# Performance work log

Hardware: AMD Instinct MI355X
Metric: run time of the kernel (lower is better)

Reference implementation:

```python
import jax, jax.numpy as jnp
import numpy as np

B, N, H, DH, M = 4, 4096, 16, 64, 266  # batch, seq, heads, dim_head, nb_features
D = H * DH                              # hidden_size = 1024
EPS_FAVOR = 1e-4
EPS_LN = 1e-5


def _gaussian_orthogonal_matrix(m, d, rng):
    # performer_pytorch gaussian_orthogonal_random_matrix, scaling=0
    nb_blocks = int(np.ceil(m / d))
    blocks = []
    for _ in range(nb_blocks):
        q, _ = np.linalg.qr(rng.standard_normal((d, d)))
        blocks.append(q.T)
    W = np.concatenate(blocks, axis=0)[:m]
    multiplier = np.linalg.norm(rng.standard_normal((m, d)), axis=1)
    return (multiplier[:, None] * W).astype(np.float32)


def setup_inputs() -> dict:
    key = jax.random.key(0)
    ks = jax.random.split(key, 6)
    s = D ** -0.5
    rng = np.random.default_rng(0)
    return {
        "hidden_states": jax.random.normal(ks[0], (B, N, D), jnp.float32),
        "Wq": jax.random.normal(ks[1], (D, D), jnp.float32) * s,
        "Wk": jax.random.normal(ks[2], (D, D), jnp.float32) * s,
        "Wv": jax.random.normal(ks[3], (D, D), jnp.float32) * s,
        "Wo": jax.random.normal(ks[4], (D, D), jnp.float32) * s,
        "bo": jnp.zeros((D,), jnp.float32),
        "proj": jnp.asarray(_gaussian_orthogonal_matrix(M, DH, rng)),  # [M, DH]
        "gamma": jnp.ones((D,), jnp.float32),
        "beta": jnp.zeros((D,), jnp.float32),
    }


def _softmax_kernel(x, proj, is_query):
    # x: [B,H,N,DH]; FAVOR+ positive random features for the softmax kernel
    dn = DH ** -0.25
    ratio = proj.shape[0] ** -0.5
    xs = x * dn
    xd = jnp.einsum('bhnd,md->bhnm', xs, proj)            # [B,H,N,M]
    diag = 0.5 * jnp.sum(xs * xs, axis=-1, keepdims=True)  # ||x||^2 / (2 sqrt(d))
    if is_query:
        stab = jnp.max(xd, axis=-1, keepdims=True)
    else:
        stab = jnp.max(xd, axis=(-2, -1), keepdims=True)
    stab = jax.lax.stop_gradient(stab)
    return ratio * (jnp.exp(xd - diag - stab) + EPS_FAVOR)


def reference(hidden_states, Wq, Wk, Wv, Wo, bo, proj, gamma, beta):
    x = hidden_states
    # qkv projections (no bias), split heads -> [B,H,N,DH]
    def heads(t):
        return t.reshape(B, N, H, DH).transpose(0, 2, 1, 3)
    q = heads(x @ Wq)
    k = heads(x @ Wk)
    v = heads(x @ Wv)

    qf = _softmax_kernel(q, proj, True)    # [B,H,N,M]
    kf = _softmax_kernel(k, proj, False)   # [B,H,N,M]

    # non-causal linear attention
    k_sum = jnp.sum(kf, axis=-2)                              # [B,H,M]
    d_inv = 1.0 / jnp.einsum('bhnm,bhm->bhn', qf, k_sum)      # [B,H,N]
    ctx = jnp.einsum('bhnm,bhnd->bhmd', kf, v)                # [B,H,M,DH]
    out = jnp.einsum('bhmd,bhnm,bhn->bhnd', ctx, qf, d_inv)   # [B,H,N,DH]

    out = out.transpose(0, 2, 1, 3).reshape(B, N, D)
    out = out @ Wo + bo

    # residual + LayerNorm
    y = x + out
    mu = jnp.mean(y, axis=-1, keepdims=True)
    var = jnp.mean((y - mu) ** 2, axis=-1, keepdims=True)
    return (y - mu) / jnp.sqrt(var + EPS_LN) * gamma + beta
```

## Files before the change

kernel.cpp:

```cpp
#include <hip/hip_runtime.h>
#include <hip/hip_bf16.h>
#include <math.h>

#define Bb 4
#define Nn 4096
#define Hh 16
#define DHh 64
#define Mm 266
#define Dd 1024
#define BHh (Bb*Hh)

#define DN_SCALE 0.35355339059327373f
#define RATIO 0.06131393394849658f
#define EPS_FAVOR 1e-4f
#define EPS_LN 1e-5f

typedef __attribute__((ext_vector_type(8))) short frag_t;
typedef __attribute__((ext_vector_type(4))) short sh4;
typedef __attribute__((ext_vector_type(4))) float f32x4;

__device__ __forceinline__ ushort f2bf(float f) {
    unsigned u = __float_as_uint(f);
    return (ushort)((u + 0x7FFFu + ((u >> 16) & 1u)) >> 16);
}
__device__ __forceinline__ float bf2f(ushort h) {
    return __uint_as_float(((unsigned)h) << 16);
}
__device__ __forceinline__ unsigned fenc(float f) {
    unsigned u = __float_as_uint(f);
    return (u & 0x80000000u) ? ~u : (u | 0x80000000u);
}
__device__ __forceinline__ float fdec(unsigned e) {
    unsigned u = (e & 0x80000000u) ? (e ^ 0x80000000u) : ~e;
    return __uint_as_float(u);
}
__device__ __forceinline__ void gld16(const void* g, void* l) {
    __builtin_amdgcn_global_load_lds((const __attribute__((address_space(1))) unsigned int*)g,
                                     (__attribute__((address_space(3))) unsigned int*)l, 16, 0, 0);
}

#define SYNC_LDS() do {                                             \
        asm volatile("s_waitcnt lgkmcnt(0)" ::: "memory");          \
        __builtin_amdgcn_sched_barrier(0);                          \
        __builtin_amdgcn_s_barrier();                               \
        __builtin_amdgcn_sched_barrier(0);                          \
    } while (0)

__global__ __launch_bounds__(256) void conv_x_kernel(const float* __restrict__ x,
                                                     ushort* __restrict__ xb) {
    size_t i = ((size_t)blockIdx.x * 256 + threadIdx.x) * 8;
    float4 f0 = *(const float4*)(x + i);
    float4 f1 = *(const float4*)(x + i + 4);
    uint4 o;
    o.x = (unsigned)f2bf(f0.x) | ((unsigned)f2bf(f0.y) << 16);
    o.y = (unsigned)f2bf(f0.z) | ((unsigned)f2bf(f0.w) << 16);
    o.z = (unsigned)f2bf(f1.x) | ((unsigned)f2bf(f1.y) << 16);
    o.w = (unsigned)f2bf(f1.z) | ((unsigned)f2bf(f1.w) << 16);
    *(uint4*)(xb + i) = o;
}

__global__ __launch_bounds__(256) void conv_wt_kernel(
    const float* __restrict__ Wq, const float* __restrict__ Wk,
    const float* __restrict__ Wv, const float* __restrict__ Wo,
    ushort* __restrict__ Tq, ushort* __restrict__ Tk,
    ushort* __restrict__ Tv, ushort* __restrict__ To) {
    const int z = blockIdx.z;
    const float* W = z == 0 ? Wq : z == 1 ? Wk : z == 2 ? Wv : Wo;
    ushort* WT = z == 0 ? Tq : z == 1 ? Tk : z == 2 ? Tv : To;
    __shared__ float tls[64][65];
    const int tid = threadIdx.x;
    const int n0 = blockIdx.x * 64, k0 = blockIdx.y * 64;
    const int r = tid >> 2, seg = tid & 3;
#pragma unroll
    for (int i = 0; i < 4; ++i) {
        float4 f = *(const float4*)(W + (size_t)(k0 + r) * 1024 + n0 + seg * 16 + i * 4);
        tls[r][seg * 16 + i * 4 + 0] = f.x;
        tls[r][seg * 16 + i * 4 + 1] = f.y;
        tls[r][seg * 16 + i * 4 + 2] = f.z;
        tls[r][seg * 16 + i * 4 + 3] = f.w;
    }
    __syncthreads();
    const int nl = tid >> 2;
#pragma unroll
    for (int i = 0; i < 16; ++i)
        WT[(size_t)(n0 + nl) * 1024 + k0 + seg * 16 + i] = f2bf(tls[seg * 16 + i][nl]);
}

__global__ __launch_bounds__(256) void conv_proj_kernel(const float* __restrict__ proj,
                                                        ushort* __restrict__ pb) {
    const int idx = blockIdx.x * 256 + threadIdx.x;
    const int m = idx >> 6, k = idx & 63;
    float v = (m < Mm) ? proj[m * 64 + k] : 0.f;
    ushort hi = f2bf(v);
    float lo = v - bf2f(hi);
    pb[m * 128 + k] = hi;
    pb[m * 128 + 64 + k] = f2bf(lo);
}

__global__ __launch_bounds__(256) void diag_kernel(const ushort* __restrict__ kb,
                                                   float* __restrict__ dg) {
    const size_t i = (size_t)blockIdx.x * 256 + threadIdx.x;
    const ushort* p = kb + i * 64;
    float s = 0.f;
#pragma unroll
    for (int seg = 0; seg < 8; ++seg) {
        frag_t a = *(const frag_t*)(p + seg * 8);
#pragma unroll
        for (int j = 0; j < 8; ++j) { float f = bf2f((ushort)a[j]); s += f * f; }
    }
    dg[i] = 0.5f * s;
}

__global__ __launch_bounds__(256) void ctx2bt_kernel(const float* __restrict__ ctx,
                                                     ushort* __restrict__ cT) {
    const int mc = blockIdx.x;
    const int bh = blockIdx.y;
    const int tid = threadIdx.x;
    __shared__ float tls[64][65];
    const int r = tid >> 2, cs = tid & 3;
    const int gm = mc * 64 + r;
#pragma unroll
    for (int i = 0; i < 4; ++i) {
        float4 f = {0.f, 0.f, 0.f, 0.f};
        if (gm < Mm) f = *(const float4*)(ctx + ((size_t)bh * Mm + gm) * 64 + cs * 16 + i * 4);
        tls[r][cs * 16 + i * 4 + 0] = f.x;
        tls[r][cs * 16 + i * 4 + 1] = f.y;
        tls[r][cs * 16 + i * 4 + 2] = f.z;
        tls[r][cs * 16 + i * 4 + 3] = f.w;
    }
    __syncthreads();
    const int d = tid >> 2, ms = tid & 3;
    unsigned hi[8], lo[8];
#pragma unroll
    for (int j = 0; j < 8; ++j) {
        float v0 = tls[ms * 16 + j * 2][d];
        float v1 = tls[ms * 16 + j * 2 + 1][d];
        ushort h0 = f2bf(v0), h1 = f2bf(v1);
        ushort l0 = f2bf(v0 - bf2f(h0)), l1 = f2bf(v1 - bf2f(h1));
        hi[j] = (unsigned)h0 | ((unsigned)h1 << 16);
        lo[j] = (unsigned)l0 | ((unsigned)l1 << 16);
    }
    size_t base = (size_t)bh * 40960 + (size_t)d * 640 + mc * 64 + ms * 16;
    uint4 a = {hi[0], hi[1], hi[2], hi[3]};
    uint4 b = {hi[4], hi[5], hi[6], hi[7]};
    uint4 c = {lo[0], lo[1], lo[2], lo[3]};
    uint4 e = {lo[4], lo[5], lo[6], lo[7]};
    *(uint4*)(cT + base) = a;
    *(uint4*)(cT + base + 8) = b;
    *(uint4*)(cT + base + 320) = c;
    *(uint4*)(cT + base + 328) = e;
}

__global__ __launch_bounds__(512, 2) void gemm256(
    const ushort* __restrict__ A,
    const ushort* __restrict__ W0, const ushort* __restrict__ W1, const ushort* __restrict__ W2,
    ushort* __restrict__ o0, ushort* __restrict__ o1, ushort* __restrict__ o2,
    const float* __restrict__ bo, const float* __restrict__ xres, float* __restrict__ yres,
    int mode)
{
    __shared__ ushort smem[65536];
    const int tid = threadIdx.x;
    const int lane = tid & 63, w = tid >> 6;
    const int q = lane >> 4, m16 = lane & 15;
    const int wm = w >> 2, wn = w & 3;
    const int row0 = blockIdx.x * 256, col0 = blockIdx.y * 256;
    const int z = blockIdx.z;
    const ushort* WT = (mode == 0) ? (z == 0 ? W0 : z == 1 ? W1 : W2) : W0;

    const int srow = tid >> 2, sseg = tid & 3;
    const int ksw = (sseg ^ ((srow >> 1) & 3)) * 8;
    const int dst = tid * 8;
    const int sq  = (q ^ ((m16 >> 1) & 3)) * 8;

#define STG(T_) do {                                                          \
        int s0_ = (2 * (T_)) & 7, s1_ = (2 * (T_) + 1) & 7;                   \
        gld16(A  + (size_t)(row0 + srow) * 1024 + (T_) * 32 + ksw,            \
              smem + s0_ * 8192 + dst);                                       \
        gld16(WT + (size_t)(col0 + srow) * 1024 + (T_) * 32 + ksw,            \
              smem + s0_ * 8192 + 4096 + dst);                                \
        gld16(A  + (size_t)(row0 + 128 + srow) * 1024 + (T_) * 32 + ksw,      \
              smem + s1_ * 8192 + dst);                                       \
        gld16(WT + (size_t)(col0 + 128 + srow) * 1024 + (T_) * 32 + ksw,      \
              smem + s1_ * 8192 + 4096 + dst);                                \
    } while (0)

    f32x4 acc[8][4];
#pragma unroll
    for (int i = 0; i < 8; ++i)
#pragma unroll
        for (int j = 0; j < 4; ++j) acc[i][j] = (f32x4){0.f, 0.f, 0.f, 0.f};

    STG(0);
    STG(1);
    STG(2);

    for (int kt = 0; kt < 32; ++kt) {
        if (kt < 30)       { asm volatile("s_waitcnt vmcnt(8)" ::: "memory"); }
        else if (kt == 30) { asm volatile("s_waitcnt vmcnt(4)" ::: "memory"); }
        else               { asm volatile("s_waitcnt vmcnt(0)" ::: "memory"); }
        __builtin_amdgcn_sched_barrier(0);
        __builtin_amdgcn_s_barrier();
        __builtin_amdgcn_sched_barrier(0);

        if (kt + 3 < 32) STG(kt + 3);

        const ushort* As_ = smem + (((2 * kt + wm) & 7) * 8192);
        const ushort* Bs_ = smem + (((2 * kt + (wn >> 1)) & 7) * 8192) + 4096;
        frag_t af[8], bf[4];
#pragma unroll
        for (int i = 0; i < 8; ++i)
            af[i] = *(const frag_t*)&As_[(i * 16 + m16) * 32 + sq];
#pragma unroll
        for (int j = 0; j < 4; ++j)
            bf[j] = *(const frag_t*)&Bs_[((wn & 1) * 64 + j * 16 + m16) * 32 + sq];

        __builtin_amdgcn_s_setprio(1);
#pragma unroll
        for (int i = 0; i < 8; ++i)
#pragma unroll
            for (int j = 0; j < 4; ++j)
                acc[i][j] = __builtin_amdgcn_mfma_f32_16x16x32_bf16(af[i], bf[j], acc[i][j], 0, 0, 0);
        __builtin_amdgcn_s_setprio(0);
    }
#undef STG

    const int b = row0 >> 12;
    if (mode == 0) {
        if (z == 2) {
#pragma unroll
            for (int i = 0; i < 8; ++i)
#pragma unroll
                for (int j = 0; j < 4; ++j) {
                    int col = col0 + wn * 64 + j * 16 + m16;
                    size_t rowbase = ((size_t)((b << 4) + (col >> 6)) * 64 + (col & 63)) * 4096;
                    int n = (row0 & 4095) + wm * 128 + i * 16 + q * 4;
                    sh4 pk;
#pragma unroll
                    for (int r = 0; r < 4; ++r) pk[r] = (short)f2bf(acc[i][j][r]);
                    *(sh4*)(o2 + rowbase + n) = pk;
                }
        } else {
            ushort* outp = (z == 0) ? o0 : o1;
#pragma unroll
            for (int c = 0; c < 4; ++c) {
                __builtin_amdgcn_s_barrier();
                if (wm == (c >> 1)) {
#pragma unroll
                    for (int i2 = 0; i2 < 4; ++i2) {
                        int i = (c & 1) * 4 + i2;
#pragma unroll
                        for (int j = 0; j < 4; ++j)
#pragma unroll
                            for (int r = 0; r < 4; ++r)
                                smem[(i2 * 16 + q * 4 + r) * 264 + wn * 64 + j * 16 + m16] =
                                    f2bf(acc[i][j][r] * DN_SCALE);
                    }
                }
                __builtin_amdgcn_s_barrier();
#pragma unroll
                for (int it = 0; it < 4; ++it) {
                    int idx = it * 512 + tid;
                    int lr = idx >> 5, ch = idx & 31;
                    frag_t v = *(const frag_t*)&smem[lr * 264 + ch * 8];
                    int n = (row0 & 4095) + c * 64 + lr;
                    int h = (col0 >> 6) + (ch >> 3);
                    int dh = (ch & 7) * 8;
                    *(frag_t*)(outp + ((size_t)((b << 4) + h) * 4096 + n) * 64 + dh) = v;
                }
            }
        }
    } else {
#pragma unroll
        for (int i = 0; i < 8; ++i)
#pragma unroll
            for (int j = 0; j < 4; ++j)
#pragma unroll
                for (int r = 0; r < 4; ++r) {
                    int row = row0 + wm * 128 + i * 16 + q * 4 + r;
                    int col = col0 + wn * 64 + j * 16 + m16;
                    size_t off = (size_t)row * 1024 + col;
                    yres[off] = acc[i][j][r] + bo[col] + xres[off];
                }
    }
}

__global__ __launch_bounds__(256) void kstab_mfma_kernel(
    const ushort* __restrict__ kb, const ushort* __restrict__ pb,
    unsigned* __restrict__ stab_enc)
{
    const int n0 = blockIdx.x * 256;
    const int bh = blockIdx.y;
    const int tid = threadIdx.x;
    const int lane = tid & 63, w = tid >> 6;
    const int q = lane >> 4, m16 = lane & 15;

    __shared__ ushort ks_s[256 * 72];
    __shared__ ushort pj_s[64 * 72];

#pragma unroll
    for (int t = 0; t < 8; ++t) {
        int idx = tid + t * 256;
        int r = idx >> 3, s = idx & 7;
        *(frag_t*)&ks_s[r * 72 + s * 8] =
            *(const frag_t*)(kb + ((size_t)bh * Nn + n0 + r) * 64 + s * 8);
    }
    __syncthreads();

    frag_t aq[4][2];
#pragma unroll
    for (int g = 0; g < 4; ++g)
#pragma unroll
        for (int s = 0; s < 2; ++s)
            aq[g][s] = *(const frag_t*)&ks_s[(w * 64 + g * 16 + m16) * 72 + s * 32 + q * 8];

    float mx = -3.0e38f;
#pragma unroll
    for (int mc = 0; mc < 5; ++mc) {
        __syncthreads();
#pragma unroll
        for (int t = 0; t < 2; ++t) {
            int idx = tid + t * 256;
            int r = idx >> 3, cc = idx & 7;
            *(frag_t*)&pj_s[r * 72 + cc * 8] =
                *(const frag_t*)(pb + ((size_t)mc * 64 + r) * 128 + cc * 8);
        }
        __syncthreads();
#pragma unroll
        for (int tm = 0; tm < 4; ++tm) {
            const int t = mc * 4 + tm;
            if (t > 16) continue;
            frag_t bh0 = *(const frag_t*)&pj_s[(tm * 16 + m16) * 72 + q * 8];
            frag_t bh1 = *(const frag_t*)&pj_s[(tm * 16 + m16) * 72 + 32 + q * 8];
            bool v = (t < 16) || (m16 < 10);
#pragma unroll
            for (int g = 0; g < 4; ++g) {
                f32x4 sa = (f32x4){0.f, 0.f, 0.f, 0.f};
                sa = __builtin_amdgcn_mfma_f32_16x16x32_bf16(aq[g][0], bh0, sa, 0, 0, 0);
                sa = __builtin_amdgcn_mfma_f32_16x16x32_bf16(aq[g][1], bh1, sa, 0, 0, 0);
                if (v) {
#pragma unroll
                    for (int r = 0; r < 4; ++r) mx = fmaxf(mx, sa[r]);
                }
            }
        }
    }
    mx = fmaxf(mx, __shfl_xor(mx, 1));
    mx = fmaxf(mx, __shfl_xor(mx, 2));
    mx = fmaxf(mx, __shfl_xor(mx, 4));
    mx = fmaxf(mx, __shfl_xor(mx, 8));
    mx = fmaxf(mx, __shfl_xor(mx, 16));
    mx = fmaxf(mx, __shfl_xor(mx, 32));
    if (lane == 0) atomicMax(stab_enc + bh, fenc(mx));
}

__global__ __launch_bounds__(256) void ctx_mfma_kernel(
    const ushort* __restrict__ kb, const ushort* __restrict__ vT,
    const ushort* __restrict__ pb, const float* __restrict__ diagk,
    const unsigned* __restrict__ stab_enc,
    float* __restrict__ ctx, float* __restrict__ ksum)
{
    const int m0 = blockIdx.x * 64;
    const int nb = blockIdx.y;
    const int bh = blockIdx.z;
    const int tid = threadIdx.x;
    const int lane = tid & 63, w = tid >> 6;
    const int q = lane >> 4, m16 = lane & 15;
    const float kst = fdec(stab_enc[bh]);

    __shared__ ushort ks_s[32 * 72];
    __shared__ ushort pj_s[64 * 136];
    __shared__ ushort kf_s[64 * 40];
    __shared__ ushort vt_s[64 * 40];
    __shared__ float  diag_s[32];

    for (int u = tid; u < 1024; u += 256) {
        int r = u >> 4, c = (u & 15) * 8;
        *(frag_t*)&pj_s[r * 136 + c] = *(const frag_t*)(pb + (size_t)(m0 + r) * 128 + c);
    }

    f32x4 acc_c[4];
#pragma unroll
    for (int j = 0; j < 4; ++j) acc_c[j] = (f32x4){0.f, 0.f, 0.f, 0.f};
    float ksacc[2] = {0.f, 0.f};

    const int tn  = w & 1;
    const int tmb = (w >> 1) * 2;

    const int srow_k = tid >> 3, sseg_k = tid & 7;
    const int srow_v = tid >> 2, sseg_v = tid & 3;
    const size_t kbase = ((size_t)bh * Nn + nb * 1024 + srow_k) * 64 + sseg_k * 8;
    const size_t vbase = ((size_t)bh * 64 + srow_v) * Nn + nb * 1024 + sseg_v * 8;
    const float* dgp = diagk + (size_t)bh * Nn + nb * 1024;

    frag_t kreg = *(const frag_t*)(kb + kbase);
    frag_t vreg = *(const frag_t*)(vT + vbase);
    float4 dreg;
    if (tid < 8) dreg = *(const float4*)(dgp + tid * 4);

    for (int t = 0; t < 32; ++t) {
        __syncthreads();
        *(frag_t*)&ks_s[srow_k * 72 + sseg_k * 8] = kreg;
        *(frag_t*)&vt_s[srow_v * 40 + sseg_v * 8] = vreg;
        if (tid < 8) *(float4*)&diag_s[tid * 4] = dreg;
        __syncthreads();
        if (t < 31) {
            kreg = *(const frag_t*)(kb + kbase + (size_t)(t + 1) * 2048);
            vreg = *(const frag_t*)(vT + vbase + (size_t)(t + 1) * 32);
            if (tid < 8) dreg = *(const float4*)(dgp + (t + 1) * 32 + tid * 4);
        }

        f32x4 sa[2];
        sa[0] = (f32x4){0.f, 0.f, 0.f, 0.f};
        sa[1] = (f32x4){0.f, 0.f, 0.f, 0.f};
#pragma unroll
        for (int s = 0; s < 2; ++s) {
            frag_t a = *(const frag_t*)&ks_s[(tn * 16 + m16) * 72 + s * 32 + q * 8];
#pragma unroll
            for (int jj = 0; jj < 2; ++jj) {
                const ushort* prow = &pj_s[((tmb + jj) * 16 + m16) * 136 + s * 32 + q * 8];
                frag_t bhi = *(const frag_t*)prow;
                frag_t blo = *(const frag_t*)(prow + 64);
                sa[jj] = __builtin_amdgcn_mfma_f32_16x16x32_bf16(a, bhi, sa[jj], 0, 0, 0);
                sa[jj] = __builtin_amdgcn_mfma_f32_16x16x32_bf16(a, blo, sa[jj], 0, 0, 0);
            }
        }

#pragma unroll
        for (int jj = 0; jj < 2; ++jj) {
            int m_l = (tmb + jj) * 16 + m16;
            bool valid = (m0 + m_l) < Mm;
            sh4 pk;
            float vsum = 0.f;
#pragma unroll
            for (int r = 0; r < 4; ++r) {
                int n_l = tn * 16 + q * 4 + r;
                float val = valid ? RATIO * (__expf(sa[jj][r] - diag_s[n_l] - kst) + EPS_FAVOR) : 0.f;
                ushort hb = f2bf(val);
                pk[r] = (short)hb;
                vsum += bf2f(hb);
            }
            ksacc[jj] += vsum;
            *(sh4*)&kf_s[m_l * 40 + tn * 16 + q * 4] = pk;
        }
        __syncthreads();

        {
            frag_t a = *(const frag_t*)&kf_s[(w * 16 + m16) * 40 + q * 8];
#pragma unroll
            for (int j = 0; j < 4; ++j) {
                frag_t b = *(const frag_t*)&vt_s[(j * 16 + m16) * 40 + q * 8];
                acc_c[j] = __builtin_amdgcn_mfma_f32_16x16x32_bf16(a, b, acc_c[j], 0, 0, 0);
            }
        }
    }

#pragma unroll
    for (int j = 0; j < 4; ++j)
#pragma unroll
        for (int r = 0; r < 4; ++r) {
            int m = m0 + w * 16 + q * 4 + r;
            if (m < Mm)
                atomicAdd(&ctx[((size_t)bh * Mm + m) * 64 + j * 16 + m16], acc_c[j][r]);
        }
#pragma unroll
    for (int jj = 0; jj < 2; ++jj) {
        float v = ksacc[jj];
        v += __shfl_xor(v, 16);
        v += __shfl_xor(v, 32);
        int m = m0 + (tmb + jj) * 16 + m16;
        if (q == 0 && m < Mm) atomicAdd(&ksum[(size_t)bh * Mm + m], v);
    }
}

__global__ __launch_bounds__(256, 3) void qout_mfma_kernel(
    const ushort* __restrict__ qb, const ushort* __restrict__ pb,
    const ushort* __restrict__ cT, const float* __restrict__ ksum,
    ushort* __restrict__ attnb)
{
    const int n0 = blockIdx.x * 64;
    const int bh = blockIdx.y;
    const int b = bh >> 4, h = bh & 15;
    const int tid = threadIdx.x;
    const int lane = tid & 63, w = tid >> 6;
    const int q = lane >> 4, m16 = lane & 15;

    __shared__ ushort qs_s[64 * 64];
    __shared__ ushort pj_s[2 * 64 * 136];
    __shared__ ushort qf_s[64 * 72];
    __shared__ float  diag_s[64];
    __shared__ float  ksum_s[320];

    const ushort* cbase = cT + (size_t)bh * 40960;

#define LOADCH(i_) {                                                              \
        for (int t_ = 0; t_ < 4; ++t_) {                                          \
            int idx_ = tid + t_ * 256, rr_ = idx_ >> 4, cc_ = idx_ & 15;          \
            g[t_] = ((i_) <= 4)                                                   \
                ? *(const frag_t*)(pb + (size_t)((i_) * 64 + rr_) * 128 + cc_ * 8)\
                : *(const frag_t*)(cbase + (size_t)rr_ * 640 + (cc_ >> 3) * 320   \
                                   + ((i_) - 5) * 64 + (cc_ & 7) * 8);            \
        } }
#define STORECH(i_) {                                                             \
        ushort* sl_ = pj_s + (((i_) & 1) * 8704);                                 \
        for (int t_ = 0; t_ < 4; ++t_) {                                          \
            int idx_ = tid + t_ * 256, rr_ = idx_ >> 4, cc_ = idx_ & 15;          \
            *(frag_t*)&sl_[rr_ * 136 + cc_ * 8] = g[t_];                          \
        } }

    for (int m = tid; m < 320; m += 256)
        ksum_s[m] = (m < Mm) ? ksum[(size_t)bh * Mm + m] : 0.f;

    const ushort* qsrc = qb + ((size_t)bh * Nn + n0) * 64;
    gld16(qsrc + tid * 8,        (void*)(qs_s + tid * 8));
    gld16(qsrc + 2048 + tid * 8, (void*)(qs_s + 2048 + tid * 8));

    frag_t g[4];
    LOADCH(0);
    STORECH(0);
    LOADCH(1);
    asm volatile("s_waitcnt vmcnt(4)" ::: "memory");
    __builtin_amdgcn_sched_barrier(0);
    SYNC_LDS();

    if (tid < 64) {
        float s = 0.f;
#pragma unroll 8
        for (int k = 0; k < 64; ++k) { float f = bf2f(qs_s[tid * 64 + k]); s += f * f; }
        diag_s[tid] = 0.5f * s;
    }
    frag_t aq[2];
#pragma unroll
    for (int s = 0; s < 2; ++s)
        aq[s] = *(const frag_t*)&qs_s[(w * 16 + m16) * 64 + s * 32 + q * 8];
    SYNC_LDS();

    f32x4 sA[20];
#pragma unroll
    for (int t = 0; t < 20; ++t) sA[t] = (f32x4){0.f, 0.f, 0.f, 0.f};

#pragma unroll
    for (int mc = 0; mc < 5; ++mc) {
        const ushort* sl = pj_s + ((mc & 1) * 8704);
        __builtin_amdgcn_s_setprio(1);
#pragma unroll
        for (int tm = 0; tm < 4; ++tm)
#pragma unroll
            for (int s = 0; s < 2; ++s) {
                const ushort* pr = &sl[(tm * 16 + m16) * 136 + s * 32 + q * 8];
                frag_t bhi = *(const frag_t*)pr;
                frag_t blo = *(const frag_t*)(pr + 64);
                sA[mc * 4 + tm] = __builtin_amdgcn_mfma_f32_16x16x32_bf16(aq[s], bhi, sA[mc * 4 + tm], 0, 0, 0);
                sA[mc * 4 + tm] = __builtin_amdgcn_mfma_f32_16x16x32_bf16(aq[s], blo, sA[mc * 4 + tm], 0, 0, 0);
            }
        __builtin_amdgcn_s_setprio(0);
        STORECH(mc + 1);
        LOADCH(mc + 2);
        SYNC_LDS();
    }

    float mx[4] = {-3.0e38f, -3.0e38f, -3.0e38f, -3.0e38f};
#pragma unroll
    for (int t = 0; t < 17; ++t) {
        bool v = (t < 16) || (m16 < 10);
        if (v) {
#pragma unroll
            for (int r = 0; r < 4; ++r) mx[r] = fmaxf(mx[r], sA[t][r]);
        }
    }
#pragma unroll
    for (int r = 0; r < 4; ++r) {
        float v = mx[r];
        v = fmaxf(v, __shfl_xor(v, 1));
        v = fmaxf(v, __shfl_xor(v, 2));
        v = fmaxf(v, __shfl_xor(v, 4));
        v = fmaxf(v, __shfl_xor(v, 8));
        mx[r] = v;
    }
    float dg[4];
#pragma unroll
    for (int r = 0; r < 4; ++r) dg[r] = diag_s[w * 16 + q * 4 + r];

    float ds[4] = {0.f, 0.f, 0.f, 0.f};
    f32x4 oA[4];
#pragma unroll
    for (int dt = 0; dt < 4; ++dt) oA[dt] = (f32x4){0.f, 0.f, 0.f, 0.f};

#pragma unroll
    for (int mc = 0; mc < 5; ++mc) {
#pragma unroll
        for (int tm = 0; tm < 4; ++tm) {
            int t = mc * 4 + tm;
            float ksm = ksum_s[t * 16 + m16];
#pragma unroll
            for (int r = 0; r < 4; ++r) {
                ushort hb = f2bf(RATIO * (__expf(sA[t][r] - dg[r] - mx[r]) + EPS_FAVOR));
                ds[r] += bf2f(hb) * ksm;
                qf_s[(w * 16 + q * 4 + r) * 72 + tm * 16 + m16] = hb;
            }
        }
        const ushort* sl = pj_s + (((mc + 5) & 1) * 8704);
        __builtin_amdgcn_s_setprio(1);
#pragma unroll
        for (int s = 0; s < 2; ++s) {
            frag_t a = *(const frag_t*)&qf_s[(w * 16 + m16) * 72 + s * 32 + q * 8];
#pragma unroll
            for (int dt = 0; dt < 4; ++dt) {
                const ushort* pr = &sl[(dt * 16 + m16) * 136 + s * 32 + q * 8];
                frag_t bhi = *(const frag_t*)pr;
                frag_t blo = *(const frag_t*)(pr + 64);
                oA[dt] = __builtin_amdgcn_mfma_f32_16x16x32_bf16(a, bhi, oA[dt], 0, 0, 0);
                oA[dt] = __builtin_amdgcn_mfma_f32_16x16x32_bf16(a, blo, oA[dt], 0, 0, 0);
            }
        }
        __builtin_amdgcn_s_setprio(0);
        if (mc + 6 <= 9) STORECH(mc + 6);
        if (mc + 7 <= 9) LOADCH(mc + 7);
        SYNC_LDS();
    }
#undef LOADCH
#undef STORECH

#pragma unroll
    for (int r = 0; r < 4; ++r) {
        float v = ds[r];
        v += __shfl_xor(v, 1);
        v += __shfl_xor(v, 2);
        v += __shfl_xor(v, 4);
        v += __shfl_xor(v, 8);
        ds[r] = 1.0f / v;
    }
#pragma unroll
    for (int dt = 0; dt < 4; ++dt)
#pragma unroll
        for (int r = 0; r < 4; ++r) {
            int n = n0 + w * 16 + q * 4 + r;
            attnb[((size_t)(b * Nn + n)) * Dd + h * 64 + dt * 16 + m16] =
                f2bf(oA[dt][r] * ds[r]);
        }
}

__global__ __launch_bounds__(256) void ln_kernel(
    const float* __restrict__ y, const float* __restrict__ gamma,
    const float* __restrict__ beta, float* __restrict__ out)
{
    const int row = blockIdx.x;
    const int tid = threadIdx.x;
    float4 v = *(const float4*)(y + (size_t)row * Dd + tid * 4);
    float s = v.x + v.y + v.z + v.w;
    float q = v.x * v.x + v.y * v.y + v.z * v.z + v.w * v.w;
    __shared__ float rs[256], rq[256];
    rs[tid] = s; rq[tid] = q;
    __syncthreads();
    for (int off = 128; off > 0; off >>= 1) {
        if (tid < off) { rs[tid] += rs[tid + off]; rq[tid] += rq[tid + off]; }
        __syncthreads();
    }
    float mu = rs[0] * (1.0f / Dd);
    float var = rq[0] * (1.0f / Dd) - mu * mu;
    float rstd = rsqrtf(var + EPS_LN);
    float4 gm = *(const float4*)(gamma + tid * 4);
    float4 bt = *(const float4*)(beta + tid * 4);
    float4 o;
    o.x = (v.x - mu) * rstd * gm.x + bt.x;
    o.y = (v.y - mu) * rstd * gm.y + bt.y;
    o.z = (v.z - mu) * rstd * gm.z + bt.z;
    o.w = (v.w - mu) * rstd * gm.w + bt.w;
    *(float4*)(out + (size_t)row * Dd + tid * 4) = o;
}

extern "C" void kernel_launch(void* const* d_in, const int* in_sizes, int n_in,
                              void* d_out, int out_size, void* d_ws, size_t ws_size,
                              hipStream_t stream) {
    const float* x     = (const float*)d_in[0];
    const float* Wq    = (const float*)d_in[1];
    const float* Wk    = (const float*)d_in[2];
    const float* Wv    = (const float*)d_in[3];
    const float* Wo    = (const float*)d_in[4];
    const float* bo    = (const float*)d_in[5];
    const float* proj  = (const float*)d_in[6];
    const float* gamma = (const float*)d_in[7];
    const float* beta  = (const float*)d_in[8];
    float* out = (float*)d_out;

    const size_t TS = 16777216;
    ushort* xb  = (ushort*)d_ws;
    ushort* qb  = xb + TS;
    ushort* kb  = qb + TS;
    ushort* vb  = kb + TS;
    ushort* WTq = vb + TS;
    ushort* WTk = WTq + 1048576;
    ushort* WTv = WTk + 1048576;
    ushort* WTo = WTv + 1048576;
    float*  ctx  = (float*)(WTo + 1048576);
    float*  ksum = ctx + (size_t)BHh * Mm * DHh;
    unsigned* stab = (unsigned*)(ksum + (size_t)BHh * Mm);
    ushort* attnb = xb;
    float*  yres  = (float*)qb;
    ushort* vT     = vb;
    float*  diagk  = (float*)WTq;
    ushort* projb2 = WTk;
    ushort* ctxT   = vb;

    hipMemsetAsync(ctx, 0, (size_t)BHh * Mm * DHh * sizeof(float), stream);
    hipMemsetAsync(ksum, 0, (size_t)BHh * Mm * sizeof(float), stream);
    hipMemsetAsync(stab, 0, BHh * sizeof(unsigned), stream);

    conv_x_kernel<<<8192, 256, 0, stream>>>(x, xb);
    conv_wt_kernel<<<dim3(16, 16, 4), 256, 0, stream>>>(Wq, Wk, Wv, Wo, WTq, WTk, WTv, WTo);

    gemm256<<<dim3(64, 4, 3), 512, 0, stream>>>(xb, WTq, WTk, WTv, qb, kb, vT,
                                                nullptr, nullptr, nullptr, 0);

    diag_kernel<<<1024, 256, 0, stream>>>(kb, diagk);
    conv_proj_kernel<<<80, 256, 0, stream>>>(proj, projb2);

    kstab_mfma_kernel<<<dim3(Nn / 256, BHh), 256, 0, stream>>>(kb, projb2, stab);

    ctx_mfma_kernel<<<dim3(5, 4, BHh), 256, 0, stream>>>(kb, vT, projb2, diagk, stab,
                                                         ctx, ksum);

    ctx2bt_kernel<<<dim3(5, BHh), 256, 0, stream>>>(ctx, ctxT);

    qout_mfma_kernel<<<dim3(Nn / 64, BHh), 256, 0, stream>>>(qb, projb2, ctxT, ksum, attnb);

    gemm256<<<dim3(64, 4, 1), 512, 0, stream>>>(attnb, WTo, nullptr, nullptr,
                                                nullptr, nullptr, nullptr, bo, x, yres, 1);
    ln_kernel<<<16384, 256, 0, stream>>>(yres, gamma, beta, out);
}
```

Measured before the change: 562.6 us.

## Double-buffer LDS fragment registers to overlap next-tile reads with MFMA

Restructures the bf16 GEMM main loop so the next k-tile's A/B fragments are read from shared memory into a second register set while MFMAs run on the current set. The loop is unrolled by two to alternate the register buffers. The global-load wait is shifted to vmcnt(4) because each step now needs the following stage to have landed. This hides LDS read latency behind matrix instructions, at the cost of roughly 48 extra VGPRs per thread, which may reduce occupancy or cause spills.

```diff
diff --git a/kernel.cpp b/kernel.cpp
--- a/kernel.cpp
+++ b/kernel.cpp
@@ -190,38 +190,58 @@
 #pragma unroll
         for (int j = 0; j < 4; ++j) acc[i][j] = (f32x4){0.f, 0.f, 0.f, 0.f};
 
+    frag_t afA[8], bfA[4], afB[8], bfB[4];
+
     STG(0);
     STG(1);
     STG(2);
 
-    for (int kt = 0; kt < 32; ++kt) {
-        if (kt < 30)       { asm volatile("s_waitcnt vmcnt(8)" ::: "memory"); }
-        else if (kt == 30) { asm volatile("s_waitcnt vmcnt(4)" ::: "memory"); }
-        else               { asm volatile("s_waitcnt vmcnt(0)" ::: "memory"); }
-        __builtin_amdgcn_sched_barrier(0);
-        __builtin_amdgcn_s_barrier();
-        __builtin_amdgcn_sched_barrier(0);
-
-        if (kt + 3 < 32) STG(kt + 3);
-
-        const ushort* As_ = smem + (((2 * kt + wm) & 7) * 8192);
-        const ushort* Bs_ = smem + (((2 * kt + (wn >> 1)) & 7) * 8192) + 4096;
-        frag_t af[8], bf[4];
+    asm volatile("s_waitcnt vmcnt(8)" ::: "memory");
+    __builtin_amdgcn_sched_barrier(0);
+    __builtin_amdgcn_s_barrier();
+    __builtin_amdgcn_sched_barrier(0);
+    {
+        const ushort* A0 = smem + ((wm & 7) * 8192);
+        const ushort* B0 = smem + (((wn >> 1) & 7) * 8192) + 4096;
 #pragma unroll
         for (int i = 0; i < 8; ++i)
-            af[i] = *(const frag_t*)&As_[(i * 16 + m16) * 32 + sq];
+            afA[i] = *(const frag_t*)&A0[(i * 16 + m16) * 32 + sq];
 #pragma unroll
         for (int j = 0; j < 4; ++j)
-            bf[j] = *(const frag_t*)&Bs_[((wn & 1) * 64 + j * 16 + m16) * 32 + sq];
-
-        __builtin_amdgcn_s_setprio(1);
-#pragma unroll
-        for (int i = 0; i < 8; ++i)
-#pragma unroll
-            for (int j = 0; j < 4; ++j)
-                acc[i][j] = __builtin_amdgcn_mfma_f32_16x16x32_bf16(af[i], bf[j], acc[i][j], 0, 0, 0);
-        __builtin_amdgcn_s_setprio(0);
-    }
+            bfA[j] = *(const frag_t*)&B0[((wn & 1) * 64 + j * 16 + m16) * 32 + sq];
+    }
+
+#define STEP(CURA, CURB, NXTA, NXTB, KT_) do {                                    \
+        if ((KT_) < 30) { asm volatile("s_waitcnt vmcnt(4)" ::: "memory"); }      \
+        else            { asm volatile("s_waitcnt vmcnt(0)" ::: "memory"); }      \
+        __builtin_amdgcn_sched_barrier(0);                                        \
+        __builtin_amdgcn_s_barrier();                                             \
+        __builtin_amdgcn_sched_barrier(0);                                        \
+        if ((KT_) + 3 < 32) STG((KT_) + 3);                                       \
+        const ushort* An_ = smem + (((2 * ((KT_) + 1) + wm) & 7) * 8192);         \
+        const ushort* Bn_ = smem + (((2 * ((KT_) + 1) + (wn >> 1)) & 7) * 8192) + 4096; \
+        __builtin_amdgcn_s_setprio(1);                                            \
+        _Pragma("unroll")                                                         \
+        for (int g = 0; g < 4; ++g) {                                             \
+            if ((KT_) + 1 < 32) {                                                 \
+                NXTA[2 * g]     = *(const frag_t*)&An_[((2 * g) * 16 + m16) * 32 + sq];     \
+                NXTA[2 * g + 1] = *(const frag_t*)&An_[((2 * g + 1) * 16 + m16) * 32 + sq]; \
+                NXTB[g]         = *(const frag_t*)&Bn_[((wn & 1) * 64 + g * 16 + m16) * 32 + sq]; \
+            }                                                                     \
+            _Pragma("unroll")                                                     \
+            for (int j = 0; j < 4; ++j) {                                         \
+                acc[2 * g][j]     = __builtin_amdgcn_mfma_f32_16x16x32_bf16(CURA[2 * g],     CURB[j], acc[2 * g][j], 0, 0, 0);     \
+                acc[2 * g + 1][j] = __builtin_amdgcn_mfma_f32_16x16x32_bf16(CURA[2 * g + 1], CURB[j], acc[2 * g + 1][j], 0, 0, 0); \
+            }                                                                     \
+        }                                                                         \
+        __builtin_amdgcn_s_setprio(0);                                            \
+    } while (0)
+
+    for (int kt = 0; kt < 32; kt += 2) {
+        STEP(afA, bfA, afB, bfB, kt);
+        STEP(afB, bfB, afA, bfA, kt + 1);
+    }
+#undef STEP
 #undef STG
 
     const int b = row0 >> 12;
```

Result: no change. 561.6 us (-0.2%).
